# Performance work log

Hardware: AMD Instinct MI355X
Metric: run time of the kernel (lower is better)

## Reference

```python
import jax, jax.numpy as jnp
import numpy as np

N = 100000      # nodes
E = 1600000     # edges
F_IN = 64       # node_features
F_OUT = 32      # output_size


def _cheb2(H, row, col, w_norm, theta, bias):
    # ChebConv K=2, sym normalization, lambda_max=2 (GCLSTM default):
    # L_hat = L - I = -D^{-1/2} A D^{-1/2}, so T0 = H, T1 = -A_norm H
    agg = jax.ops.segment_sum(w_norm[:, None] * H[col], row, num_segments=N)  # [N, F_OUT]
    return H @ theta[0] - agg @ theta[1] + bias


def setup_inputs() -> dict:
    key = jax.random.key(0)
    ks = jax.random.split(key, 24)
    inp = {}
    inp["x"] = jax.random.normal(ks[0], (N, F_IN), jnp.float32)
    inp["edge_index"] = jax.random.randint(ks[1], (2, E), 0, N)
    inp["edge_weight"] = jax.random.uniform(ks[2], (E,), jnp.float32)
    inp["h"] = jax.random.normal(ks[3], (N, F_OUT), jnp.float32)
    inp["c"] = jax.random.normal(ks[4], (N, F_OUT), jnp.float32)
    s_in = float(1.0 / np.sqrt(F_IN))
    s_out = float(1.0 / np.sqrt(F_OUT))
    i = 5
    for g in "ifco":
        inp[f"W_{g}"] = jax.random.uniform(ks[i], (F_IN, F_OUT), jnp.float32, -s_in, s_in); i += 1
        inp[f"b_{g}"] = jax.random.uniform(ks[i], (1, F_OUT), jnp.float32, -s_in, s_in); i += 1
        inp[f"theta_{g}"] = jax.random.uniform(ks[i], (2, F_OUT, F_OUT), jnp.float32, -s_out, s_out); i += 1
        inp[f"cb_{g}"] = jax.random.uniform(ks[i], (F_OUT,), jnp.float32, -s_out, s_out); i += 1
    inp["W_lin"] = jax.random.uniform(ks[i], (F_OUT, 1), jnp.float32, -s_out, s_out); i += 1
    inp["b_lin"] = jax.random.uniform(ks[i], (1,), jnp.float32, -s_out, s_out)
    return inp


def reference(x, edge_index, edge_weight, h, c,
              W_i, b_i, theta_i, cb_i,
              W_f, b_f, theta_f, cb_f,
              W_c, b_c, theta_c, cb_c,
              W_o, b_o, theta_o, cb_o,
              W_lin, b_lin):
    row, col = edge_index[0], edge_index[1]
    # symmetric normalization of edge weights (get_laplacian 'sym')
    deg = jax.ops.segment_sum(edge_weight, row, num_segments=N)
    dis = jnp.where(deg > 0, jax.lax.rsqrt(jnp.where(deg > 0, deg, 1.0)), 0.0)
    w_norm = dis[row] * edge_weight * dis[col]  # [E]
    # GCLSTM gates: input x through dense W, hidden h through ChebConv
    I = jax.nn.sigmoid(x @ W_i + _cheb2(h, row, col, w_norm, theta_i, cb_i) + b_i)
    Fg = jax.nn.sigmoid(x @ W_f + _cheb2(h, row, col, w_norm, theta_f, cb_f) + b_f)
    T = jnp.tanh(x @ W_c + _cheb2(h, row, col, w_norm, theta_c, cb_c) + b_c)
    C = Fg * c + I * T
    O = jax.nn.sigmoid(x @ W_o + _cheb2(h, row, col, w_norm, theta_o, cb_o) + b_o)
    H = O * jnp.tanh(C)
    # wrapper head: relu then Linear(out, 1)
    return jax.nn.relu(H) @ W_lin + b_lin  # [N, 1]
```

## Files before the change

### kernel.cpp

```cpp
#include <hip/hip_runtime.h>
#include <math.h>

#define NN 100000
#define NE 1600000
#define BSH 7
#define BMSK 127
#define NBUK 782
#define CAP 2560
#define NSB 391
#define EPC 4096
#define CAPH 1536

typedef __attribute__((ext_vector_type(8))) short bf16x8;
typedef __attribute__((ext_vector_type(4))) float f32x4;

#define MFMA(A, B, C) __builtin_amdgcn_mfma_f32_16x16x32_bf16(A, B, C, 0, 0, 0)

__device__ __forceinline__ float fsigm(float z) { return 1.0f / (1.0f + __expf(-z)); }
__device__ __forceinline__ float ftanh(float z) { return 1.0f - 2.0f / (__expf(2.0f * z) + 1.0f); }

__device__ __forceinline__ void split1(float v, unsigned short* hi, unsigned short* lo) {
  unsigned u = __float_as_uint(v);
  *hi = (unsigned short)(u >> 16);
  float hf = __uint_as_float(u & 0xFFFF0000u);
  float lf = v - hf;
  *lo = (unsigned short)(__float_as_uint(lf) >> 16);
}

__device__ __forceinline__ void split8(const float* f, bf16x8* hi, bf16x8* lo) {
#pragma unroll
  for (int j = 0; j < 8; ++j) {
    unsigned short h, l;
    split1(f[j], &h, &l);
    (*hi)[j] = (short)h;
    (*lo)[j] = (short)l;
  }
}

__device__ __forceinline__ bf16x8 as_bf16x8(uint4 q) {
  union { uint4 q; bf16x8 v; } u;
  u.q = q;
  return u.v;
}

__device__ __forceinline__ void load8(const float4* p, int idx4, float* f) {
  float4 a = p[idx4];
  float4 b = p[idx4 + 1];
  f[0] = a.x; f[1] = a.y; f[2] = a.z; f[3] = a.w;
  f[4] = b.x; f[5] = b.y; f[6] = b.z; f[7] = b.w;
}


__global__ __launch_bounds__(256) void k_scat(const int* __restrict__ row,
                                              const int* __restrict__ col,
                                              const float* __restrict__ ew,
                                              int* __restrict__ cursor,
                                              int2* __restrict__ colw) {
  __shared__ int hist[NBUK];
  const int t = threadIdx.x;
  const int bid = blockIdx.x;
  for (int i = t; i < NBUK; i += 256) hist[i] = 0;
  __syncthreads();
  const int e0 = bid * EPC;
  const int e1 = min(e0 + EPC, NE);
  for (int e = e0 + t; e < e1; e += 256)
    atomicAdd(&hist[row[e] >> BSH], 1);
  __syncthreads();
  const int off = (bid * 61) % NBUK;
  for (int i0 = t; i0 < NBUK; i0 += 256) {
    int i = i0 + off;
    if (i >= NBUK) i -= NBUK;
    int h = hist[i];
    if (h > 0) hist[i] = atomicAdd(&cursor[i], h);
  }
  __syncthreads();
  for (int e = e0 + t; e < e1; e += 256) {
    int r = row[e];
    int c = col[e];
    float w = ew[e];
    int b = r >> BSH;
    int slot = atomicAdd(&hist[b], 1);
    if (slot < CAP)
      colw[b * CAP + slot] = make_int2(c | ((r & BMSK) << 17), __float_as_int(w));
  }
}

struct DegParams {
  const int* cursor;
  const int2* colw;
  float* dis;
  const float* W[4];
  const float* T0[4];
  const float* T1[4];
  const float* bsrc[4];
  const float* cb[4];
  uint4* fh;
  uint4* fl;
  float* bias;
};

__global__ __launch_bounds__(256) void k_deg(DegParams p) {
  const int t = threadIdx.x;
  const int bid = blockIdx.x;
  if (bid >= NBUK) {
    int ex = bid - NBUK;
    if (ex < 8) {
      int idx = ex * 256 + t;
      int T = idx >> 6;
      int lane = idx & 63;
      int ncol = ((T & 7) * 16) + (lane & 15);
      int g = ncol >> 5;
      int c = ncol & 31;
      int kq = (lane >> 4) * 8;
      const float* mat;
      int kbase;
      if (T < 16) { mat = p.W[g]; kbase = (T >> 3) * 32 + kq; }
      else if (T < 24) { mat = p.T0[g]; kbase = kq; }
      else { mat = p.T1[g]; kbase = kq; }
      unsigned hw[4], lw[4];
#pragma unroll
      for (int jj = 0; jj < 4; ++jj) {
        unsigned short h0, l0, h1, l1;
        split1(mat[(kbase + 2 * jj) * 32 + c], &h0, &l0);
        split1(mat[(kbase + 2 * jj + 1) * 32 + c], &h1, &l1);
        hw[jj] = (unsigned)h0 | ((unsigned)h1 << 16);
        lw[jj] = (unsigned)l0 | ((unsigned)l1 << 16);
      }
      p.fh[idx] = make_uint4(hw[0], hw[1], hw[2], hw[3]);
      p.fl[idx] = make_uint4(lw[0], lw[1], lw[2], lw[3]);
    } else if (t < 128) {
      p.bias[t] = p.bsrc[t >> 5][t & 31] + p.cb[t >> 5][t & 31];
    }
    return;
  }
  __shared__ float dg[128];
  if (t < 128) dg[t] = 0.0f;
  __syncthreads();
  const int M = min(p.cursor[bid], CAP);
  const int base = bid * CAP;
  for (int i = t; i < M; i += 256) {
    int2 e = p.colw[base + i];
    atomicAdd(&dg[e.x >> 17], __int_as_float(e.y));
  }
  __syncthreads();
  int node = (bid << BSH) + t;
  if (t < 128 && node < NN) {
    float d = dg[t];
    p.dis[node] = d > 0.0f ? rsqrtf(d) : 0.0f;
  }
}

struct FusedParams {
  const float4* x4;
  const float4* h4;
  const float* cst;
  const int* cursor;
  const int2* colw;
  const float* dis;
  const uint4* fh;
  const uint4* fl;
  const float* bias;
  const float* wlin;
  const float* blin;
  float* out;
};

__global__ __launch_bounds__(256) void k_fused(FusedParams p) {
  __shared__ int2 stage[CAPH];
  __shared__ int cnt[64], excl[64], cur64[64];
  __shared__ int s[256];
  const int t = threadIdx.x;
  const int jb = blockIdx.x;
  const int b = jb >> 1;
  const int hf = jb & 1;
  const int nbase = (b << BSH) + (hf << 6);
  if (nbase >= NN) return;
  if (t < 64) cnt[t] = 0;
  __syncthreads();

  const int base = b * CAP;
  const int M = min(p.cursor[b], CAP);
  for (int i = t; i < M; i += 256) {
    int rl = p.colw[base + i].x >> 17;
    if ((rl >> 6) == hf) atomicAdd(&cnt[rl & 63], 1);
  }
  __syncthreads();
  {
    int v = (t < 64) ? cnt[t] : 0;
    s[t] = v;
    __syncthreads();
    for (int o = 1; o < 64; o <<= 1) {
      int a = (t >= o) ? s[t - o] : 0;
      __syncthreads();
      s[t] += a;
      __syncthreads();
    }
    if (t < 64) {
      excl[t] = s[t] - v;
      cur64[t] = s[t] - v;
    }
  }
  __syncthreads();
  for (int i = t; i < M; i += 256) {
    int2 e = p.colw[base + i];
    int rl = e.x >> 17;
    if ((rl >> 6) == hf) {
      int c = e.x & 0x1FFFF;
      float w = __int_as_float(e.y) * p.dis[c];
      int slot = atomicAdd(&cur64[rl & 63], 1);
      if (slot < CAPH) stage[slot] = make_int2(c, __float_as_int(w));
    }
  }
  __syncthreads();

  const int lane = t & 63;
  const int wv = t >> 6;
  const int mr = lane & 15;
  const int quad = lane >> 4;
  const int m0 = nbase + wv * 16;
  int m = m0 + mr;
  if (m >= NN) m = NN - 1;
  const int rlh = m - nbase;

  bf16x8 xh[2], xl[2], hh, hl, gh, gl;
  float f[8];
#pragma unroll
  for (int kt = 0; kt < 2; ++kt) {
    load8(p.x4, (m * 64 + kt * 32 + quad * 8) >> 2, f);
    split8(f, &xh[kt], &xl[kt]);
  }
  load8(p.h4, (m * 32 + quad * 8) >> 2, f);
  split8(f, &hh, &hl);

  float fa[8] = {0.f, 0.f, 0.f, 0.f, 0.f, 0.f, 0.f, 0.f};
  float fb[8] = {0.f, 0.f, 0.f, 0.f, 0.f, 0.f, 0.f, 0.f};
  {
    int s0 = excl[rlh];
    int rem = cnt[rlh];
    int j = 0;
    for (; j + 3 < rem; j += 4) {
      int2 w0 = stage[s0 + j], w1 = stage[s0 + j + 1];
      int2 w2 = stage[s0 + j + 2], w3 = stage[s0 + j + 3];
      const float4* h0 = p.h4 + (w0.x * 8 + quad * 2);
      const float4* h1 = p.h4 + (w1.x * 8 + quad * 2);
      const float4* h2 = p.h4 + (w2.x * 8 + quad * 2);
      const float4* h3 = p.h4 + (w3.x * 8 + quad * 2);
      float4 a0 = h0[0], a1 = h0[1];
      float4 b0 = h1[0], b1 = h1[1];
      float4 c0 = h2[0], c1 = h2[1];
      float4 d0 = h3[0], d1 = h3[1];
      float f0 = __int_as_float(w0.y), f1 = __int_as_float(w1.y);
      float f2 = __int_as_float(w2.y), f3 = __int_as_float(w3.y);
      fa[0] = fmaf(f0, a0.x, fa[0]); fa[1] = fmaf(f0, a0.y, fa[1]);
      fa[2] = fmaf(f0, a0.z, fa[2]); fa[3] = fmaf(f0, a0.w, fa[3]);
      fa[4] = fmaf(f0, a1.x, fa[4]); fa[5] = fmaf(f0, a1.y, fa[5]);
      fa[6] = fmaf(f0, a1.z, fa[6]); fa[7] = fmaf(f0, a1.w, fa[7]);
      fb[0] = fmaf(f1, b0.x, fb[0]); fb[1] = fmaf(f1, b0.y, fb[1]);
      fb[2] = fmaf(f1, b0.z, fb[2]); fb[3] = fmaf(f1, b0.w, fb[3]);
      fb[4] = fmaf(f1, b1.x, fb[4]); fb[5] = fmaf(f1, b1.y, fb[5]);
      fb[6] = fmaf(f1, b1.z, fb[6]); fb[7] = fmaf(f1, b1.w, fb[7]);
      fa[0] = fmaf(f2, c0.x, fa[0]); fa[1] = fmaf(f2, c0.y, fa[1]);
      fa[2] = fmaf(f2, c0.z, fa[2]); fa[3] = fmaf(f2, c0.w, fa[3]);
      fa[4] = fmaf(f2, c1.x, fa[4]); fa[5] = fmaf(f2, c1.y, fa[5]);
      fa[6] = fmaf(f2, c1.z, fa[6]); fa[7] = fmaf(f2, c1.w, fa[7]);
      fb[0] = fmaf(f3, d0.x, fb[0]); fb[1] = fmaf(f3, d0.y, fb[1]);
      fb[2] = fmaf(f3, d0.z, fb[2]); fb[3] = fmaf(f3, d0.w, fb[3]);
      fb[4] = fmaf(f3, d1.x, fb[4]); fb[5] = fmaf(f3, d1.y, fb[5]);
      fb[6] = fmaf(f3, d1.z, fb[6]); fb[7] = fmaf(f3, d1.w, fb[7]);
    }
    for (; j < rem; ++j) {
      int2 cw = stage[s0 + j];
      const float4* hp = p.h4 + (cw.x * 8 + quad * 2);
      float4 a0 = hp[0], a1 = hp[1];
      float w = __int_as_float(cw.y);
      fa[0] = fmaf(w, a0.x, fa[0]); fa[1] = fmaf(w, a0.y, fa[1]);
      fa[2] = fmaf(w, a0.z, fa[2]); fa[3] = fmaf(w, a0.w, fa[3]);
      fa[4] = fmaf(w, a1.x, fa[4]); fa[5] = fmaf(w, a1.y, fa[5]);
      fa[6] = fmaf(w, a1.z, fa[6]); fa[7] = fmaf(w, a1.w, fa[7]);
    }
  }
  {
    float dn = -p.dis[m];
#pragma unroll
    for (int j = 0; j < 8; ++j) f[j] = dn * (fa[j] + fb[j]);
    split8(f, &gh, &gl);
  }

  float wl0 = p.wlin[mr];
  float wl1 = p.wlin[mr + 16];
  float bl = p.blin[0];

  f32x4 acc[8];
#pragma unroll 2
  for (int nt = 0; nt < 8; ++nt) {
    float bv = p.bias[nt * 16 + mr];
    f32x4 a;
    a[0] = bv; a[1] = bv; a[2] = bv; a[3] = bv;
    bf16x8 b0h = as_bf16x8(p.fh[nt * 64 + lane]);
    bf16x8 b0l = as_bf16x8(p.fl[nt * 64 + lane]);
    bf16x8 b1h = as_bf16x8(p.fh[(8 + nt) * 64 + lane]);
    bf16x8 b1l = as_bf16x8(p.fl[(8 + nt) * 64 + lane]);
    bf16x8 t0h = as_bf16x8(p.fh[(16 + nt) * 64 + lane]);
    bf16x8 t0l = as_bf16x8(p.fl[(16 + nt) * 64 + lane]);
    bf16x8 t1h = as_bf16x8(p.fh[(24 + nt) * 64 + lane]);
    bf16x8 t1l = as_bf16x8(p.fl[(24 + nt) * 64 + lane]);
    a = MFMA(xh[0], b0h, a); a = MFMA(xh[0], b0l, a); a = MFMA(xl[0], b0h, a);
    a = MFMA(xh[1], b1h, a); a = MFMA(xh[1], b1l, a); a = MFMA(xl[1], b1h, a);
    a = MFMA(hh, t0h, a);    a = MFMA(hh, t0l, a);    a = MFMA(hl, t0h, a);
    a = MFMA(gh, t1h, a);    a = MFMA(gh, t1l, a);    a = MFMA(gl, t1h, a);
    acc[nt] = a;
  }

#pragma unroll
  for (int r = 0; r < 4; ++r) {
    int node = m0 + quad * 4 + r;
    int nc = node < NN ? node : NN - 1;
    float c0 = p.cst[nc * 32 + mr];
    float c1 = p.cst[nc * 32 + 16 + mr];
    float I0 = fsigm(acc[0][r]), I1 = fsigm(acc[1][r]);
    float F0 = fsigm(acc[2][r]), F1 = fsigm(acc[3][r]);
    float T0 = ftanh(acc[4][r]), T1 = ftanh(acc[5][r]);
    float O0 = fsigm(acc[6][r]), O1 = fsigm(acc[7][r]);
    float C0 = fmaf(F0, c0, I0 * T0);
    float C1 = fmaf(F1, c1, I1 * T1);
    float H0 = O0 * ftanh(C0);
    float H1 = O1 * ftanh(C1);
    float part = fmaf(fmaxf(H0, 0.f), wl0, fmaxf(H1, 0.f) * wl1);
#pragma unroll
    for (int sh = 1; sh < 16; sh <<= 1) part += __shfl_xor(part, sh, 64);
    if (mr == 0 && node < NN) p.out[node] = part + bl;
  }
}

extern "C" void kernel_launch(void* const* d_in, const int* in_sizes, int n_in,
                              void* d_out, int out_size, void* d_ws, size_t ws_size,
                              hipStream_t stream) {
  const float* x = (const float*)d_in[0];
  const int* row = (const int*)d_in[1];
  const int* col = row + NE;
  const float* ew = (const float*)d_in[2];
  const float* h = (const float*)d_in[3];
  const float* c = (const float*)d_in[4];

  float* ws = (float*)d_ws;
  float* dis = ws;
  int* cursor = (int*)(ws + 100000);
  uint4* fh = (uint4*)(ws + 100800);
  uint4* fl = (uint4*)(ws + 108992);
  float* biasws = ws + 117184;
  int2* colw = (int2*)(ws + 117312);

  hipMemsetAsync(cursor, 0, NBUK * sizeof(int), stream);
  k_scat<<<NSB, 256, 0, stream>>>(row, col, ew, cursor, colw);

  DegParams dp;
  dp.cursor = cursor;
  dp.colw = colw;
  dp.dis = dis;
  for (int g = 0; g < 4; ++g) {
    dp.W[g] = (const float*)d_in[5 + 4 * g];
    dp.bsrc[g] = (const float*)d_in[6 + 4 * g];
    dp.T0[g] = (const float*)d_in[7 + 4 * g];
    dp.T1[g] = dp.T0[g] + 1024;
    dp.cb[g] = (const float*)d_in[8 + 4 * g];
  }
  dp.fh = fh;
  dp.fl = fl;
  dp.bias = biasws;
  k_deg<<<NBUK + 9, 256, 0, stream>>>(dp);

  FusedParams fp;
  fp.x4 = (const float4*)x;
  fp.h4 = (const float4*)h;
  fp.cst = c;
  fp.cursor = cursor;
  fp.colw = colw;
  fp.dis = dis;
  fp.fh = fh;
  fp.fl = fl;
  fp.bias = biasws;
  fp.wlin = (const float*)d_in[21];
  fp.blin = (const float*)d_in[22];
  fp.out = (float*)d_out;
  k_fused<<<2 * NBUK, 256, 0, stream>>>(fp);
}
```

Measured before the change: 260.6 us.

## Stage scattered edges in shared memory by bucket before global write

The edge-bucketing kernel now computes a block-local exclusive prefix sum over bucket counts and first places the packed edges into a shared-memory staging array sorted by bucket. A second pass writes them to global memory in staging order, so consecutive threads store to contiguous slots within each bucket rather than to random buckets. This aims to coalesce the global scatter writes. The cost is about 40KB of extra LDS per block, which lowers occupancy, plus an extra scan and barriers.

```diff
diff --git a/kernel.cpp b/kernel.cpp
--- a/kernel.cpp
+++ b/kernel.cpp
@@ -56,32 +56,74 @@
                                               const float* __restrict__ ew,
                                               int* __restrict__ cursor,
                                               int2* __restrict__ colw) {
-  __shared__ int hist[NBUK];
+  __shared__ int cnt[NBUK];
+  __shared__ int excl[NBUK];
+  __shared__ int gbase[NBUK];
+  __shared__ int2 stage[EPC];
+  __shared__ unsigned short lbuk[EPC];
+  __shared__ int s[256];
   const int t = threadIdx.x;
   const int bid = blockIdx.x;
-  for (int i = t; i < NBUK; i += 256) hist[i] = 0;
+  for (int i = t; i < NBUK; i += 256) cnt[i] = 0;
   __syncthreads();
   const int e0 = bid * EPC;
   const int e1 = min(e0 + EPC, NE);
+  const int M = e1 - e0;
   for (int e = e0 + t; e < e1; e += 256)
-    atomicAdd(&hist[row[e] >> BSH], 1);
-  __syncthreads();
-  const int off = (bid * 61) % NBUK;
-  for (int i0 = t; i0 < NBUK; i0 += 256) {
-    int i = i0 + off;
-    if (i >= NBUK) i -= NBUK;
-    int h = hist[i];
-    if (h > 0) hist[i] = atomicAdd(&cursor[i], h);
-  }
+    atomicAdd(&cnt[row[e] >> BSH], 1);
+  __syncthreads();
+  {
+    int loc[4];
+    int sum = 0;
+#pragma unroll
+    for (int k = 0; k < 4; ++k) {
+      int i = t * 4 + k;
+      int v = (i < NBUK) ? cnt[i] : 0;
+      loc[k] = sum;
+      sum += v;
+    }
+    s[t] = sum;
+    __syncthreads();
+    for (int o = 1; o < 256; o <<= 1) {
+      int a = (t >= o) ? s[t - o] : 0;
+      __syncthreads();
+      s[t] += a;
+      __syncthreads();
+    }
+    int ex = s[t] - sum;
+#pragma unroll
+    for (int k = 0; k < 4; ++k) {
+      int i = t * 4 + k;
+      if (i < NBUK) excl[i] = ex + loc[k];
+    }
+  }
+  __syncthreads();
+  {
+    const int off = (bid * 61) % NBUK;
+    for (int i0 = t; i0 < NBUK; i0 += 256) {
+      int i = i0 + off;
+      if (i >= NBUK) i -= NBUK;
+      int h = cnt[i];
+      gbase[i] = (h > 0) ? atomicAdd(&cursor[i], h) : 0;
+    }
+  }
+  __syncthreads();
+  for (int i = t; i < NBUK; i += 256) cnt[i] = excl[i];
   __syncthreads();
   for (int e = e0 + t; e < e1; e += 256) {
     int r = row[e];
     int c = col[e];
     float w = ew[e];
     int b = r >> BSH;
-    int slot = atomicAdd(&hist[b], 1);
-    if (slot < CAP)
-      colw[b * CAP + slot] = make_int2(c | ((r & BMSK) << 17), __float_as_int(w));
+    int slot = atomicAdd(&cnt[b], 1);
+    stage[slot] = make_int2(c | ((r & BMSK) << 17), __float_as_int(w));
+    lbuk[slot] = (unsigned short)b;
+  }
+  __syncthreads();
+  for (int i = t; i < M; i += 256) {
+    int b = lbuk[i];
+    int pos = gbase[b] + (i - excl[b]);
+    if (pos < CAP) colw[b * CAP + pos] = stage[i];
   }
 }
 
```

Result: faster. 245.3 us (-5.9%).
